# Kernel tuning notes

Measured on AMD Instinct MI355X. Metric: run time of the kernel, lower is better.

## Reference

```python
import jax, jax.numpy as jnp
import numpy as np
from functools import partial

EPS = 1e-12  # F.normalize eps (clamp_min on the norm)


def conv2d(x, w, b, groups=1):
    # x: [B, Cin, H, W], w: [Cout, Cin//groups, 3, 3], 'same' padding, stride 1
    y = jax.lax.conv_general_dilated(
        x, w, window_strides=(1, 1), padding='SAME',
        dimension_numbers=('NCHW', 'OIHW', 'NCHW'),
        feature_group_count=groups)
    return y + b[None, :, None, None]


def setup_inputs() -> dict:
    key = jax.random.key(0)
    ks = jax.random.split(key, 8)
    B, C, H, W = 16, 256, 32, 32
    HW = H * W
    T = 2  # tasks: seg, depth
    return {
        'features_seg': jax.random.normal(ks[0], (B, C, H, W), jnp.float32),
        'features_depth': jax.random.normal(ks[1], (B, C, H, W), jnp.float32),
        'proj_w_seg': jax.random.normal(ks[2], (C, C, 3, 3), jnp.float32) * 0.02,
        'proj_b_seg': jnp.zeros((C,), jnp.float32),
        'proj_w_depth': jax.random.normal(ks[3], (C, C, 3, 3), jnp.float32) * 0.02,
        'proj_b_depth': jnp.zeros((C,), jnp.float32),
        'fusion_w': jax.random.normal(ks[4], (HW, T, 3, 3), jnp.float32) * 0.02,
        'fusion_b': jnp.zeros((HW,), jnp.float32),
    }


def reference(features_seg, features_depth, proj_w_seg, proj_b_seg,
              proj_w_depth, proj_b_depth, fusion_w, fusion_b):
    gamma = 0.5
    feats = [features_seg, features_depth]
    proj = [(proj_w_seg, proj_b_seg), (proj_w_depth, proj_b_depth)]
    B, C, H, W = features_seg.shape
    HW = H * W

    # Per-task cosine-similarity affinity matrices [B, HW, HW]
    Ms = []
    for f in feats:
        fv = f.reshape(B, C, HW)
        fn = fv / jnp.maximum(jnp.linalg.norm(fv, axis=1, keepdims=True), EPS)
        aff = jnp.einsum('bci,bcj->bij', fn, fn)  # [B, HW, HW]
        Ms.append(aff.reshape(B, HW, H, W))

    # Stack on dim=2 then flatten -> interleaved channels [B, HW*T, H, W]
    M = jnp.stack(Ms, axis=2).reshape(B, -1, H, W)
    M = conv2d(M, fusion_w, fusion_b, groups=HW)  # [B, HW, H, W]

    attention = M.reshape(B, HW, HW).transpose(0, 2, 1)  # [B, HW, HW]

    outs = []
    for f, (w, b) in zip(feats, proj):
        value = conv2d(f, w, b).reshape(B, C, HW)          # [B, C, HW]
        attended = jnp.einsum('bck,bkj->bcj', value, attention)
        attended = attended.reshape(B, C, H, W)
        outs.append(gamma * attended + (1.0 - gamma) * f)
    return tuple(outs)
```

## Files before the change

### kernel.cpp

```cpp
#include <hip/hip_runtime.h>
#include <hip/hip_bf16.h>

typedef __bf16 bf16;
typedef __attribute__((ext_vector_type(8))) __bf16 bf16x8;
typedef __attribute__((ext_vector_type(4))) __bf16 bf16x4v;
typedef __attribute__((ext_vector_type(4))) float f32x4;

#define B_  16
#define C_  256
#define HW_ 1024
#define PADR 1156
#define ZSTR 295936

__device__ __forceinline__ void gll16(const bf16* g, bf16* l) {
  __builtin_amdgcn_global_load_lds((const __attribute__((address_space(1))) void*)g,
                                   (__attribute__((address_space(3))) void*)l, 16, 0, 0);
}

__global__ void prep_fat(const float* __restrict__ f0, const float* __restrict__ f1,
                         const float* __restrict__ w0, const float* __restrict__ w1,
                         bf16* __restrict__ fTpad, float* __restrict__ rn,
                         bf16* __restrict__ Wr) {
  int tid = threadIdx.x;
  if (blockIdx.x >= 1024) {
    int i = (blockIdx.x - 1024) * 256 + tid;
    int t = i / 589824, r2 = i % 589824;
    int c = r2 / 2304, r = r2 % 2304;
    int cin = r / 9, d = r % 9;
    Wr[(size_t)t * 589824 + c * 2304 + d * 256 + cin] = (bf16)(t ? w1 : w0)[r2];
    return;
  }
  __shared__ float sm[256][33];
  __shared__ float ps[8][32];
  int bx = blockIdx.x & 31, z = blockIdx.x >> 5;
  int t = z >> 4, b = z & 15;
  int k0 = bx * 32;
  const float* fb = (t ? f1 : f0) + (size_t)b * C_ * HW_ + k0;
  int kk = tid & 31, cg = tid >> 5;
  float ssq = 0.f;
  #pragma unroll
  for (int i = 0; i < 32; ++i) {
    int c = cg + i * 8;
    float v = fb[(size_t)c * HW_ + kk];
    sm[c][kk] = v;
    ssq += v * v;
  }
  ps[cg][kk] = ssq;

  bf16x8 zv;
  #pragma unroll
  for (int e = 0; e < 8; ++e) zv[e] = (bf16)0.f;
  if (tid < 64) {
    int c = (tid & 31) * 8, side = tid >> 5;
    *(bf16x8*)(fTpad + ((size_t)z * PADR + (bx + 1) * 34 + side * 33) * C_ + c) = zv;
  }
  if (bx == 0 || bx == 31) {
    int prow = (bx == 0) ? 0 : 33;
    for (int q = tid; q < 34 * 32; q += 256) {
      int wcol = q >> 5, c = (q & 31) * 8;
      *(bf16x8*)(fTpad + ((size_t)z * PADR + prow * 34 + wcol) * C_ + c) = zv;
    }
  }

  __syncthreads();
  if (tid < 32) {
    float s = 0.f;
    #pragma unroll
    for (int r = 0; r < 8; ++r) s += ps[r][tid];
    rn[z * 1024 + k0 + tid] = 1.f / fmaxf(sqrtf(s), 1e-12f);
  }
  int wl = tid >> 3, c0 = (tid & 7) * 32;
  bf16* dst = fTpad + ((size_t)z * PADR + (bx + 1) * 34 + wl + 1) * C_ + c0;
  #pragma unroll
  for (int u = 0; u < 4; ++u) {
    bf16x8 vv;
    #pragma unroll
    for (int e = 0; e < 8; ++e) vv[e] = (bf16)sm[c0 + u * 8 + e][wl];
    *(bf16x8*)(dst + u * 8) = vv;
  }
}

__global__ void fusion_conv2(const bf16* __restrict__ aff, const float* __restrict__ fw,
                             const float* __restrict__ fb, bf16* __restrict__ M) {
  __shared__ float sa[2][1024];
  int bi = blockIdx.x;
  int i = bi & 1023, b = bi >> 10;
  int tid = threadIdx.x;
  #pragma unroll
  for (int t = 0; t < 2; ++t) {
    const bf16* arow = aff + (((size_t)t * 16 + b) * 1024 + i) * 1024;
    bf16x4v ch = ((const bf16x4v*)arow)[tid];
    sa[t][tid * 4 + 0] = (float)ch[0];
    sa[t][tid * 4 + 1] = (float)ch[1];
    sa[t][tid * 4 + 2] = (float)ch[2];
    sa[t][tid * 4 + 3] = (float)ch[3];
  }
  float wgt[2][9];
  #pragma unroll
  for (int t = 0; t < 2; ++t)
    #pragma unroll
    for (int q = 0; q < 9; ++q) wgt[t][q] = fw[i * 18 + t * 9 + q];
  float bias = fb[i];
  __syncthreads();
  #pragma unroll
  for (int s0 = 0; s0 < 4; ++s0) {
    int s = tid + s0 * 256;
    int h = s >> 5, w = s & 31;
    float acc = bias;
    #pragma unroll
    for (int kh = 0; kh < 3; ++kh) {
      int hh = h + kh - 1;
      if ((unsigned)hh < 32u) {
        #pragma unroll
        for (int kw = 0; kw < 3; ++kw) {
          int ww = w + kw - 1;
          if ((unsigned)ww < 32u) {
            acc += wgt[0][kh * 3 + kw] * sa[0][hh * 32 + ww];
            acc += wgt[1][kh * 3 + kw] * sa[1][hh * 32 + ww];
          }
        }
      }
    }
    M[((size_t)bi << 10) + s] = (bf16)acc;
  }
}

template<int MODE>
__device__ __forceinline__
void gemm_core(int bx, int by, int z, bf16* As, bf16* Bs,
               const bf16* __restrict__ A, long long sA,
               const bf16* __restrict__ Bm, long long sB, int K,
               bf16* __restrict__ Cb, long long sC,
               const float* __restrict__ x0, const float* __restrict__ x1,
               float* __restrict__ Co) {
  const int tt = (MODE == 1) ? (z >> 4) : (z & 1);
  const int bb = (MODE == 1) ? (z & 15) : (z >> 1);
  const int zold = tt * 16 + bb;
  const bf16* Ab = A + (size_t)(MODE == 3 ? tt : z) * sA;
  const bf16* Bb = Bm + (size_t)(MODE == 1 ? z : (MODE == 2 ? bb : zold)) * sB;
  const int m0 = by * 128, n0 = bx * 128;
  const int tid = threadIdx.x;
  const int lane = tid & 63, wave = tid >> 6;
  const int wm = (wave >> 1) * 64, wn = (wave & 1) * 64;
  const int fr = lane & 15, fq = lane >> 4;

  const bf16* srcA[4];
  const bf16* srcB[4];
  int ldsA[4], ldsB[4];
  #pragma unroll
  for (int s = 0; s < 4; ++s) {
    int q = (wave * 4 + s) * 64 + lane;
    int row = q >> 3, c = (q & 7) ^ (row & 7);
    ldsA[s] = ldsB[s] = __builtin_amdgcn_readfirstlane((wave * 4 + s) * 512);
    if (MODE == 1) {
      int j = m0 + row;
      srcA[s] = Ab + (size_t)(((j >> 5) + 1) * 34 + (j & 31) + 1) * C_ + c * 8;
    } else {
      srcA[s] = Ab + (size_t)(m0 + row) * K + c * 8;
    }
    int jb = n0 + row;
    if (MODE == 1 || MODE == 3) {
      srcB[s] = Bb + (size_t)(((jb >> 5) + 1) * 34 + (jb & 31) + 1) * C_ + c * 8;
    } else {
      srcB[s] = Bb + (size_t)jb * K + c * 8;
    }
  }
  int lA[2][4], lB[2][4];
  #pragma unroll
  for (int h = 0; h < 2; ++h) {
    #pragma unroll
    for (int i = 0; i < 4; ++i) {
      int rr = wm + i * 16 + fr;
      lA[h][i] = rr * 64 + (((h * 4) + fq) ^ (rr & 7)) * 8;
      int rc = wn + i * 16 + fr;
      lB[h][i] = rc * 64 + (((h * 4) + fq) ^ (rc & 7)) * 8;
    }
  }

  f32x4 acc[4][4];
  #pragma unroll
  for (int i = 0; i < 4; ++i)
    #pragma unroll
    for (int j = 0; j < 4; ++j) acc[i][j] = 0.f;

  for (int k0 = 0; k0 < K; k0 += 64) {
    int boff;
    if (MODE == 3) {
      int d = k0 >> 8;
      int kh = d / 3, kw = d % 3;
      boff = ((kh - 1) * 34 + (kw - 1)) * C_ + (k0 & 255);
    } else {
      boff = k0;
    }
    #pragma unroll
    for (int s = 0; s < 4; ++s) gll16(srcA[s] + k0, As + ldsA[s]);
    #pragma unroll
    for (int s = 0; s < 4; ++s) gll16(srcB[s] + boff, Bs + ldsB[s]);
    __syncthreads();
    #pragma unroll
    for (int h = 0; h < 2; ++h) {
      bf16x8 af[4], bfr[4];
      #pragma unroll
      for (int i = 0; i < 4; ++i) af[i] = *(const bf16x8*)(&As[lA[h][i]]);
      #pragma unroll
      for (int j = 0; j < 4; ++j) bfr[j] = *(const bf16x8*)(&Bs[lB[h][j]]);
      #pragma unroll
      for (int i = 0; i < 4; ++i)
        #pragma unroll
        for (int j = 0; j < 4; ++j)
          acc[i][j] = __builtin_amdgcn_mfma_f32_16x16x32_bf16(af[i], bfr[j], acc[i][j], 0, 0, 0);
    }
    __syncthreads();
  }

  #pragma unroll
  for (int i = 0; i < 4; ++i) {
    int rbase = m0 + wm + i * 16 + fq * 4;
    #pragma unroll
    for (int j = 0; j < 4; ++j) {
      int col = n0 + wn + j * 16 + fr;
      float cj = (MODE == 1) ? x0[(size_t)z * 1024 + col] : 0.f;
      #pragma unroll
      for (int r = 0; r < 4; ++r) {
        int row = rbase + r;
        float v = acc[i][j][r];
        if (MODE == 1) {
          Cb[(size_t)z * sC + (size_t)row * 1024 + col] =
              (bf16)(v * x0[(size_t)z * 1024 + row] * cj);
        } else if (MODE == 3) {
          const float* bias = tt ? x1 : x0;
          Cb[(size_t)z * sC + (size_t)row * 1024 + col] = (bf16)(v + bias[row]);
        } else {
          const float* fp = tt ? x1 : x0;
          Co[(size_t)zold * sC + (size_t)row * 1024 + col] =
              0.5f * v + 0.5f * fp[(size_t)bb * sC + (size_t)row * 1024 + col];
        }
      }
    }
  }
}

__global__ __launch_bounds__(256, 4)
void gemm_fat(const bf16* __restrict__ fTpad, const float* __restrict__ rn,
              bf16* __restrict__ aff, const bf16* __restrict__ Wr,
              bf16* __restrict__ value, const float* __restrict__ b0,
              const float* __restrict__ b1) {
  __shared__ bf16 As[128 * 64];
  __shared__ bf16 Bs[128 * 64];
  int blk = blockIdx.x;
  if (blk < 2048) {
    gemm_core<1>(blk & 7, (blk >> 3) & 7, blk >> 6, As, Bs,
                 fTpad, ZSTR, fTpad, ZSTR, C_,
                 aff, (long long)HW_ * HW_, rn, rn, nullptr);
  } else {
    int q = blk - 2048;
    gemm_core<3>(q & 7, (q >> 3) & 1, q >> 4, As, Bs,
                 Wr, 589824LL, fTpad, ZSTR, 2304,
                 value, (long long)C_ * HW_, b0, b1, nullptr);
  }
}

__global__ __launch_bounds__(256, 4)
void gemm_attend(const bf16* __restrict__ value, const bf16* __restrict__ Mbuf,
                 const float* __restrict__ f0, const float* __restrict__ f1,
                 float* __restrict__ out) {
  __shared__ bf16 As[128 * 64];
  __shared__ bf16 Bs[128 * 64];
  gemm_core<2>(blockIdx.x, blockIdx.y, blockIdx.z, As, Bs,
               value, (long long)C_ * HW_, Mbuf, (long long)HW_ * HW_, 1024,
               nullptr, (long long)C_ * HW_, f0, f1, out);
}

extern "C" void kernel_launch(void* const* d_in, const int* in_sizes, int n_in,
                              void* d_out, int out_size, void* d_ws, size_t ws_size,
                              hipStream_t stream) {
  const float* f0 = (const float*)d_in[0];
  const float* f1 = (const float*)d_in[1];
  const float* w0 = (const float*)d_in[2];
  const float* b0 = (const float*)d_in[3];
  const float* w1 = (const float*)d_in[4];
  const float* b1 = (const float*)d_in[5];
  const float* fusion_w = (const float*)d_in[6];
  const float* fusion_b = (const float*)d_in[7];
  float* out = (float*)d_out;

  char* ws = (char*)d_ws;
  bf16* aff   = (bf16*)ws;
  bf16* Mbuf  = (bf16*)ws;
  bf16* fTpad = (bf16*)(ws + 67108864ull);
  bf16* Wr    = (bf16*)(ws + 86048768ull);
  bf16* value = (bf16*)(ws + 88408064ull);
  float* rn   = (float*)(ws + 105185280ull);

  prep_fat<<<5632, 256, 0, stream>>>(f0, f1, w0, w1, fTpad, rn, Wr);
  gemm_fat<<<2560, 256, 0, stream>>>(fTpad, rn, aff, Wr, value, b0, b1);
  fusion_conv2<<<16384, 256, 0, stream>>>(aff, fusion_w, fusion_b, Mbuf);
  gemm_attend<<<dim3(8, 2, 32), 256, 0, stream>>>(value, Mbuf, f0, f1, out);
}
```

Baseline: 247.0 us.

## Exploit affinity symmetry: compute upper-triangle tiles and mirror via LDS transpose

The affinity GEMM now launches only the upper-triangular 128x128 tiles, 36 of 64 per batch-task. Each off-diagonal tile stages its result in LDS and writes the transposed copy to the mirrored position, cutting the affinity MFMA work by about 44%. The fused launch is split into separate affinity and value-projection kernels. This adds a larger LDS footprint (128x133 bf16, about 34 KB), which may lower occupancy, plus an extra sync and a strided LDS transpose pass.

```diff
diff --git a/kernel.cpp b/kernel.cpp
--- a/kernel.cpp
+++ b/kernel.cpp
@@ -11,6 +11,7 @@
 #define HW_ 1024
 #define PADR 1156
 #define ZSTR 295936
+#define TP  133
 
 __device__ __forceinline__ void gll16(const bf16* g, bf16* l) {
   __builtin_amdgcn_global_load_lds((const __attribute__((address_space(1))) void*)g,
@@ -127,7 +128,7 @@
 
 template<int MODE>
 __device__ __forceinline__
-void gemm_core(int bx, int by, int z, bf16* As, bf16* Bs,
+void gemm_core(int bx, int by, int z, bf16* As, bf16* Bs, bf16* T,
                const bf16* __restrict__ A, long long sA,
                const bf16* __restrict__ Bm, long long sB, int K,
                bf16* __restrict__ Cb, long long sC,
@@ -213,6 +214,7 @@
     __syncthreads();
   }
 
+  const bool mirror = (MODE == 1) && (bx != by);
   #pragma unroll
   for (int i = 0; i < 4; ++i) {
     int rbase = m0 + wm + i * 16 + fq * 4;
@@ -225,8 +227,9 @@
         int row = rbase + r;
         float v = acc[i][j][r];
         if (MODE == 1) {
-          Cb[(size_t)z * sC + (size_t)row * 1024 + col] =
-              (bf16)(v * x0[(size_t)z * 1024 + row] * cj);
+          bf16 sv = (bf16)(v * x0[(size_t)z * 1024 + row] * cj);
+          Cb[(size_t)z * sC + (size_t)row * 1024 + col] = sv;
+          if (mirror) T[(row - m0) * TP + (col - n0)] = sv;
         } else if (MODE == 3) {
           const float* bias = tt ? x1 : x0;
           Cb[(size_t)z * sC + (size_t)row * 1024 + col] = (bf16)(v + bias[row]);
@@ -238,35 +241,48 @@
       }
     }
   }
+  if (mirror) {
+    __syncthreads();
+    #pragma unroll
+    for (int s = 0; s < 8; ++s) {
+      int q2 = s * 256 + tid;
+      int g = q2 >> 4, c0 = (q2 & 15) << 3;
+      bf16x8 vv;
+      #pragma unroll
+      for (int e = 0; e < 8; ++e) vv[e] = T[(c0 + e) * TP + g];
+      *(bf16x8*)(Cb + (size_t)z * sC + (size_t)(n0 + g) * 1024 + m0 + c0) = vv;
+    }
+  }
 }
 
 __global__ __launch_bounds__(256, 4)
-void gemm_fat(const bf16* __restrict__ fTpad, const float* __restrict__ rn,
-              bf16* __restrict__ aff, const bf16* __restrict__ Wr,
-              bf16* __restrict__ value, const float* __restrict__ b0,
-              const float* __restrict__ b1) {
-  __shared__ bf16 As[128 * 64];
-  __shared__ bf16 Bs[128 * 64];
-  int blk = blockIdx.x;
-  if (blk < 2048) {
-    gemm_core<1>(blk & 7, (blk >> 3) & 7, blk >> 6, As, Bs,
-                 fTpad, ZSTR, fTpad, ZSTR, C_,
-                 aff, (long long)HW_ * HW_, rn, rn, nullptr);
-  } else {
-    int q = blk - 2048;
-    gemm_core<3>(q & 7, (q >> 3) & 1, q >> 4, As, Bs,
-                 Wr, 589824LL, fTpad, ZSTR, 2304,
-                 value, (long long)C_ * HW_, b0, b1, nullptr);
-  }
+void gemm_aff(const bf16* __restrict__ fTpad, const float* __restrict__ rn,
+              bf16* __restrict__ aff) {
+  __shared__ bf16 smem[128 * TP];
+  int q = blockIdx.x, by = 0, cnt = 8;
+  while (q >= cnt) { q -= cnt; ++by; --cnt; }
+  int bx = by + q;
+  gemm_core<1>(bx, by, blockIdx.z, smem, smem + 8192, smem,
+               fTpad, ZSTR, fTpad, ZSTR, C_,
+               aff, (long long)HW_ * HW_, rn, rn, nullptr);
+}
+
+__global__ __launch_bounds__(256, 4)
+void gemm_value(const bf16* __restrict__ Wr, const bf16* __restrict__ fTpad,
+                bf16* __restrict__ value, const float* __restrict__ b0,
+                const float* __restrict__ b1) {
+  __shared__ bf16 smem[128 * 128];
+  gemm_core<3>(blockIdx.x, blockIdx.y, blockIdx.z, smem, smem + 8192, smem,
+               Wr, 589824LL, fTpad, ZSTR, 2304,
+               value, (long long)C_ * HW_, b0, b1, nullptr);
 }
 
 __global__ __launch_bounds__(256, 4)
 void gemm_attend(const bf16* __restrict__ value, const bf16* __restrict__ Mbuf,
                  const float* __restrict__ f0, const float* __restrict__ f1,
                  float* __restrict__ out) {
-  __shared__ bf16 As[128 * 64];
-  __shared__ bf16 Bs[128 * 64];
-  gemm_core<2>(blockIdx.x, blockIdx.y, blockIdx.z, As, Bs,
+  __shared__ bf16 smem[128 * 128];
+  gemm_core<2>(blockIdx.x, blockIdx.y, blockIdx.z, smem, smem + 8192, smem,
                value, (long long)C_ * HW_, Mbuf, (long long)HW_ * HW_, 1024,
                nullptr, (long long)C_ * HW_, f0, f1, out);
 }
@@ -293,7 +309,8 @@
   float* rn   = (float*)(ws + 105185280ull);
 
   prep_fat<<<5632, 256, 0, stream>>>(f0, f1, w0, w1, fTpad, rn, Wr);
-  gemm_fat<<<2560, 256, 0, stream>>>(fTpad, rn, aff, Wr, value, b0, b1);
+  gemm_aff<<<dim3(36, 1, 32), 256, 0, stream>>>(fTpad, rn, aff);
+  gemm_value<<<dim3(8, 2, 32), 256, 0, stream>>>(Wr, fTpad, value, b0, b1);
   fusion_conv2<<<16384, 256, 0, stream>>>(aff, fusion_w, fusion_b, Mbuf);
   gemm_attend<<<dim3(8, 2, 32), 256, 0, stream>>>(value, Mbuf, f0, f1, out);
 }
```

New measurement: 233.2 us. -5.6%, faster.
